# Performance work log

Hardware: AMD Instinct MI355X
Metric: run time of the kernel (lower is better)

The kernel has to match this reference:

```python
import jax, jax.numpy as jnp
import numpy as np

N = 100_000      # nodes
E = 1_600_000    # edges (avg degree 16)
D_IN, D_H, D_OUT = 128, 128, 64


def setup_inputs() -> dict:
    key = jax.random.key(0)
    ks = jax.random.split(key, 6)
    x = jax.random.normal(ks[0], (N, D_IN), jnp.float32)
    edge_index = jax.random.randint(ks[1], (2, E), 0, N, dtype=jnp.int32)
    W1 = jax.random.normal(ks[2], (D_IN, D_H), jnp.float32) / np.sqrt(D_IN)
    b1 = jnp.zeros((D_H,), jnp.float32)
    W2 = jax.random.normal(ks[3], (D_H, D_OUT), jnp.float32) / np.sqrt(D_H)
    b2 = jnp.zeros((D_OUT,), jnp.float32)
    return {"x": x, "edge_index": edge_index, "W1": W1, "b1": b1, "W2": W2, "b2": b2}


def _gcn_layer(x, W, b, src, dst, n_nodes):
    # PyG GCNConv: h = x @ W; symmetric norm with self-loops; scatter-add; + bias
    h = x @ W                                        # [N, D_out]
    deg = jax.ops.segment_sum(jnp.ones_like(dst, jnp.float32), dst,
                              num_segments=n_nodes)  # self-loops => deg >= 1
    dinv = jax.lax.rsqrt(deg)                        # deg^{-1/2}
    norm = dinv[src] * dinv[dst]                     # [E+N]
    msg = h[src] * norm[:, None]                     # gather + scale
    out = jax.ops.segment_sum(msg, dst, num_segments=n_nodes)  # scatter-add
    return out + b


def reference(x, edge_index, W1, b1, W2, b2):
    n = x.shape[0]
    loop = jnp.arange(n, dtype=edge_index.dtype)
    src = jnp.concatenate([edge_index[0], loop])     # add self-loops
    dst = jnp.concatenate([edge_index[1], loop])
    h = _gcn_layer(x, W1, b1, src, dst, n)
    h = jax.nn.relu(h)
    # dropout(p=0.5) is identity in eval mode
    out = _gcn_layer(h, W2, b2, src, dst, n)
    return out
```

## Files before the change

kernel.cpp:

```cpp
#include <hip/hip_runtime.h>
#include <hip/hip_bf16.h>


#define NTHREADS 256
#define BSH 9
#define NBMAX 256

typedef unsigned int uint;
typedef unsigned short ushort;
typedef __attribute__((ext_vector_type(8))) short short8;
typedef __attribute__((ext_vector_type(4))) float floatx4;

__device__ __forceinline__ uint pack_bf16(float a, float b) {
    __hip_bfloat162 h = __float22bfloat162_rn(make_float2(a, b));
    return *reinterpret_cast<uint*>(&h);
}
__device__ __forceinline__ float bf16_lo(uint q) { return __uint_as_float(q << 16); }
__device__ __forceinline__ float bf16_hi(uint q) { return __uint_as_float(q & 0xffff0000u); }

__global__ __launch_bounds__(256) void bucket_hist_kernel(
    const int* __restrict__ dst, int* __restrict__ bcnt, int e, int nb) {
    __shared__ int hist[NBMAX];
    int t = threadIdx.x;
    for (int b = t; b < nb; b += 256) hist[b] = 0;
    __syncthreads();
    int e0 = blockIdx.x * 2048;
#pragma unroll
    for (int v = 0; v < 2; v++) {
        int gi = e0 + t * 8 + v * 4;
        if (gi + 3 < e) {
            int4 d4 = *(const int4*)&dst[gi];
            atomicAdd(&hist[d4.x >> BSH], 1);
            atomicAdd(&hist[d4.y >> BSH], 1);
            atomicAdd(&hist[d4.z >> BSH], 1);
            atomicAdd(&hist[d4.w >> BSH], 1);
        } else {
            for (int j = 0; j < 4; j++)
                if (gi + j < e) atomicAdd(&hist[dst[gi + j] >> BSH], 1);
        }
    }
    __syncthreads();
    for (int b = t; b < nb; b += 256) {
        int v = hist[b];
        if (v) atomicAdd(&bcnt[b], v);
    }
}

__global__ void bucket_scan(const int* __restrict__ bcnt, int* __restrict__ bstart,
                            int* __restrict__ bcursor, int nb) {
    __shared__ int buf[NBMAX];
    int t = threadIdx.x;
    int v = (t < nb) ? bcnt[t] : 0;
    buf[t] = v;
    __syncthreads();
    int x = v;
    for (int off = 1; off < NBMAX; off <<= 1) {
        int y = (t >= off) ? buf[t - off] : 0;
        __syncthreads();
        x += y;
        buf[t] = x;
        __syncthreads();
    }
    if (t < nb) {
        bstart[t] = x - v;
        bcursor[t] = x - v;
    }
}

__global__ __launch_bounds__(256) void partition_kernel(
    const int* __restrict__ src, const int* __restrict__ dst,
    int* __restrict__ bcursor, int2* __restrict__ staged, int e, int nb) {
    __shared__ int eS[2048];
    __shared__ int eD[2048];
    __shared__ int hist[NBMAX];
    __shared__ int base[NBMAX];
    int t = threadIdx.x;
    int e0 = blockIdx.x * 2048;

    for (int b = t; b < nb; b += 256) hist[b] = 0;
    __syncthreads();
#pragma unroll
    for (int v = 0; v < 2; v++) {
        int li = t * 8 + v * 4;
        int gi = e0 + li;
        int4 s4, d4;
        if (gi + 3 < e) {
            s4 = *(const int4*)&src[gi];
            d4 = *(const int4*)&dst[gi];
        } else {
            const int* sp = &src[gi];
            const int* dp = &dst[gi];
            s4.x = (gi + 0 < e) ? sp[0] : 0;  d4.x = (gi + 0 < e) ? dp[0] : -1;
            s4.y = (gi + 1 < e) ? sp[1] : 0;  d4.y = (gi + 1 < e) ? dp[1] : -1;
            s4.z = (gi + 2 < e) ? sp[2] : 0;  d4.z = (gi + 2 < e) ? dp[2] : -1;
            s4.w = (gi + 3 < e) ? sp[3] : 0;  d4.w = (gi + 3 < e) ? dp[3] : -1;
        }
        *(int4*)&eS[li] = s4;
        *(int4*)&eD[li] = d4;
        if (d4.x >= 0) atomicAdd(&hist[d4.x >> BSH], 1);
        if (d4.y >= 0) atomicAdd(&hist[d4.y >> BSH], 1);
        if (d4.z >= 0) atomicAdd(&hist[d4.z >> BSH], 1);
        if (d4.w >= 0) atomicAdd(&hist[d4.w >> BSH], 1);
    }
    __syncthreads();
    for (int b = t; b < nb; b += 256) {
        int v = hist[b];
        base[b] = v ? atomicAdd(&bcursor[b], v) : 0;
        hist[b] = 0;
    }
    __syncthreads();
#pragma unroll
    for (int i = 0; i < 8; i++) {
        int li = t + i * 256;
        int d = eD[li];
        if (d >= 0) {
            int b = d >> BSH;
            int r = atomicAdd(&hist[b], 1);
            staged[base[b] + r] = make_int2(eS[li], d);
        }
    }
}

__global__ __launch_bounds__(256) void fine_count_kernel(
    const int2* __restrict__ staged, const int* __restrict__ bstart,
    const int* __restrict__ bcnt, int4* __restrict__ meta,
    int* __restrict__ startA, float* __restrict__ dinv, int n) {
    __shared__ int lcnt[512];
    __shared__ int tsum[256];
    int b = blockIdx.x;
    int t = threadIdx.x;
    lcnt[t] = 0;
    lcnt[t + 256] = 0;
    __syncthreads();
    int s0 = bstart[b];
    int m = bcnt[b];
    for (int i = t; i < m; i += 256)
        atomicAdd(&lcnt[staged[s0 + i].y & 511], 1);
    __syncthreads();
    int v0 = lcnt[2 * t];
    int v1 = lcnt[2 * t + 1];
    int tot = v0 + v1;
    tsum[t] = tot;
    __syncthreads();
    int x = tot;
    for (int off = 1; off < 256; off <<= 1) {
        int y = (t >= off) ? tsum[t - off] : 0;
        __syncthreads();
        x += y;
        tsum[t] = x;
        __syncthreads();
    }
    int excl = x - tot;
    int node = (b << BSH) + 2 * t;
    if (node < n) {
        float di = rsqrtf((float)v0 + 1.0f);
        startA[node] = s0 + excl;
        dinv[node] = di;
        meta[node] = make_int4(s0 + excl, v0, __float_as_int(di * di), 0);
    }
    if (node + 1 < n) {
        float di = rsqrtf((float)v1 + 1.0f);
        startA[node + 1] = s0 + excl + v0;
        dinv[node + 1] = di;
        meta[node + 1] = make_int4(s0 + excl + v0, v1, __float_as_int(di * di), 0);
    }
}

__global__ __launch_bounds__(256) void fine_fill_kernel(
    const int2* __restrict__ staged, const int* __restrict__ bstart,
    const int* __restrict__ bcnt, const int* __restrict__ startA,
    const float* __restrict__ dinv, int2* __restrict__ rec, int n) {
    __shared__ int lcur[512];
    __shared__ float ldv[512];
    int b = blockIdx.x;
    int t = threadIdx.x;
    int nb0 = b << BSH;
    for (int i = t; i < 512; i += 256) {
        int node = nb0 + i;
        lcur[i] = (node < n) ? startA[node] : 0;
        ldv[i] = (node < n) ? dinv[node] : 0.f;
    }
    __syncthreads();
    int s0 = bstart[b];
    int m = bcnt[b];
    for (int i = t; i < m; i += 256) {
        int2 ed = staged[s0 + i];
        int li = ed.y & 511;
        int pos = atomicAdd(&lcur[li], 1);
        float nw = dinv[ed.x] * ldv[li];
        rec[pos] = make_int2(ed.x, __float_as_int(nw));
    }
}

template <int COLS, bool XF32>
__global__ __launch_bounds__(256) void gemm_mfma(const void* __restrict__ Xv,
                                                 const float* __restrict__ W,
                                                 uint* __restrict__ Cq, int n) {
    __shared__ ushort sX[64 * 128];
    __shared__ ushort sWT[COLS * 128];
    int t = threadIdx.x;
    int rbase = blockIdx.x * 64;

    if (XF32) {
        const float* X = (const float*)Xv;
#pragma unroll
        for (int i = 0; i < 8; i++) {
            int f = t + 256 * i;
            int r = f >> 5;
            int c4 = f & 31;
            float4 v = make_float4(0.f, 0.f, 0.f, 0.f);
            int gr = rbase + r;
            if (gr < n) v = *(const float4*)(X + (size_t)gr * 128 + c4 * 4);
            uint lo = pack_bf16(v.x, v.y);
            uint hi = pack_bf16(v.z, v.w);
            int chunk = c4 >> 1;
            int sub = (c4 & 1) * 4;
            int off = r * 128 + (((chunk ^ (r & 15)) << 3) + sub);
            *(uint2*)&sX[off] = make_uint2(lo, hi);
        }
    } else {
        const ushort* X = (const ushort*)Xv;
#pragma unroll
        for (int i = 0; i < 4; i++) {
            int f = t + 256 * i;
            int r = f >> 4;
            int chunk = f & 15;
            uint4 v = make_uint4(0, 0, 0, 0);
            int gr = rbase + r;
            if (gr < n) v = *(const uint4*)(X + (size_t)gr * 128 + chunk * 8);
            int off = r * 128 + ((chunk ^ (r & 15)) << 3);
            *(uint4*)&sX[off] = v;
        }
    }
    {
        constexpr int UNITS = 64 * (COLS / 4);
        constexpr int PER_T = UNITS / 256;
#pragma unroll
        for (int i = 0; i < PER_T; i++) {
            int u = t + 256 * i;
            int kp = u / (COLS / 4);
            int n4 = u % (COLS / 4);
            int k = kp * 2;
            float4 w0 = *(const float4*)(W + (size_t)k * COLS + n4 * 4);
            float4 w1 = *(const float4*)(W + (size_t)(k + 1) * COLS + n4 * 4);
            int chunk = k >> 3;
            int sub = k & 7;
            const float* a0 = (const float*)&w0;
            const float* a1 = (const float*)&w1;
#pragma unroll
            for (int j = 0; j < 4; j++) {
                int nn = n4 * 4 + j;
                uint pk = pack_bf16(a0[j], a1[j]);
                int off = nn * 128 + (((chunk ^ (nn & 15)) << 3) + sub);
                *(uint*)&sWT[off] = pk;
            }
        }
    }
    __syncthreads();

    int lane = t & 63;
    int wave = t >> 6;
    int m = lane & 15;
    int q = lane >> 4;
    int r0 = wave * 16;

    floatx4 acc[COLS / 16];
#pragma unroll
    for (int c = 0; c < COLS / 16; c++) acc[c] = (floatx4){0.f, 0.f, 0.f, 0.f};

#pragma unroll
    for (int ks = 0; ks < 4; ks++) {
        int rr = r0 + m;
        int ca = (ks * 4 + q) ^ (rr & 15);
        short8 afrag = *(const short8*)&sX[rr * 128 + (ca << 3)];
#pragma unroll
        for (int c = 0; c < COLS / 16; c++) {
            int nn = c * 16 + m;
            int cb = (ks * 4 + q) ^ (nn & 15);
            short8 bfrag = *(const short8*)&sWT[nn * 128 + (cb << 3)];
            acc[c] = __builtin_amdgcn_mfma_f32_16x16x32_bf16(bfrag, afrag, acc[c], 0, 0, 0);
        }
    }

    int gr = rbase + r0 + m;
    if (gr < n) {
#pragma unroll
        for (int c = 0; c < COLS / 16; c++) {
            uint2 pk;
            pk.x = pack_bf16(acc[c][0], acc[c][1]);
            pk.y = pack_bf16(acc[c][2], acc[c][3]);
            *(uint2*)&Cq[(size_t)gr * (COLS / 2) + c * 8 + q * 2] = pk;
        }
    }
}

__global__ __launch_bounds__(256) void aggregate128q(
    const uint* __restrict__ hq, const int2* __restrict__ rec,
    const int4* __restrict__ meta, const float* __restrict__ bias,
    uint* __restrict__ outq, int n) {
    int w = (int)((blockIdx.x * blockDim.x + threadIdx.x) >> 5);
    if (w >= n) return;
    int fl = threadIdx.x & 31;
    const uint2* h2 = (const uint2*)hq;

    int4 mt = meta[w];
    int j0 = mt.x;
    int deg = mt.y;
    float swq = __int_as_float(mt.z);

    uint2 qs = h2[(size_t)w * 32 + fl];
    float a0 = bf16_lo(qs.x) * swq, a1 = bf16_hi(qs.x) * swq;
    float a2 = bf16_lo(qs.y) * swq, a3 = bf16_hi(qs.y) * swq;

    const int2* rp = rec + j0;
    int t = 0;
    for (; t + 8 <= deg; t += 8) {
        uint2 q[8]; float wf[8];
#pragma unroll
        for (int u = 0; u < 8; u++) {
            int2 e = rp[t + u];
            wf[u] = __int_as_float(e.y);
            q[u] = h2[(size_t)e.x * 32 + fl];
        }
#pragma unroll
        for (int u = 0; u < 8; u++) {
            a0 += bf16_lo(q[u].x) * wf[u]; a1 += bf16_hi(q[u].x) * wf[u];
            a2 += bf16_lo(q[u].y) * wf[u]; a3 += bf16_hi(q[u].y) * wf[u];
        }
    }
    for (; t + 2 <= deg; t += 2) {
        int2 e0 = rp[t], e1 = rp[t + 1];
        float w0 = __int_as_float(e0.y), w1 = __int_as_float(e1.y);
        uint2 q0 = h2[(size_t)e0.x * 32 + fl];
        uint2 q1 = h2[(size_t)e1.x * 32 + fl];
        a0 += bf16_lo(q0.x) * w0 + bf16_lo(q1.x) * w1;
        a1 += bf16_hi(q0.x) * w0 + bf16_hi(q1.x) * w1;
        a2 += bf16_lo(q0.y) * w0 + bf16_lo(q1.y) * w1;
        a3 += bf16_hi(q0.y) * w0 + bf16_hi(q1.y) * w1;
    }
    if (t < deg) {
        int2 e = rp[t];
        float wv = __int_as_float(e.y);
        uint2 q = h2[(size_t)e.x * 32 + fl];
        a0 += bf16_lo(q.x) * wv; a1 += bf16_hi(q.x) * wv;
        a2 += bf16_lo(q.y) * wv; a3 += bf16_hi(q.y) * wv;
    }

    float4 bb = *(const float4*)&bias[4 * fl];
    float o0 = fmaxf(a0 + bb.x, 0.f);
    float o1 = fmaxf(a1 + bb.y, 0.f);
    float o2 = fmaxf(a2 + bb.z, 0.f);
    float o3 = fmaxf(a3 + bb.w, 0.f);
    uint2 pk;
    pk.x = pack_bf16(o0, o1);
    pk.y = pack_bf16(o2, o3);
    *(uint2*)&outq[(size_t)w * 64 + fl * 2] = pk;
}

__global__ __launch_bounds__(256) void aggregate64q(
    const ushort* __restrict__ hq, const int2* __restrict__ rec,
    const int4* __restrict__ meta, const float* __restrict__ bias,
    float* __restrict__ out, int n) {
    int w = (int)((blockIdx.x * blockDim.x + threadIdx.x) >> 5);
    if (w >= n) return;
    int fl = threadIdx.x & 31;
    const uint* h2 = (const uint*)hq;

    int4 mt = meta[w];
    int j0 = mt.x;
    int deg = mt.y;
    float swq = __int_as_float(mt.z);

    uint qs = h2[(size_t)w * 32 + fl];
    float a0 = bf16_lo(qs) * swq;
    float a1 = bf16_hi(qs) * swq;

    const int2* rp = rec + j0;
    int t = 0;
    for (; t + 8 <= deg; t += 8) {
        uint q[8]; float wf[8];
#pragma unroll
        for (int u = 0; u < 8; u++) {
            int2 e = rp[t + u];
            wf[u] = __int_as_float(e.y);
            q[u] = h2[(size_t)e.x * 32 + fl];
        }
#pragma unroll
        for (int u = 0; u < 8; u++) {
            a0 += bf16_lo(q[u]) * wf[u];
            a1 += bf16_hi(q[u]) * wf[u];
        }
    }
    for (; t + 2 <= deg; t += 2) {
        int2 e0 = rp[t], e1 = rp[t + 1];
        float w0 = __int_as_float(e0.y), w1 = __int_as_float(e1.y);
        uint q0 = h2[(size_t)e0.x * 32 + fl];
        uint q1 = h2[(size_t)e1.x * 32 + fl];
        a0 += bf16_lo(q0) * w0 + bf16_lo(q1) * w1;
        a1 += bf16_hi(q0) * w0 + bf16_hi(q1) * w1;
    }
    if (t < deg) {
        int2 e = rp[t];
        float wv = __int_as_float(e.y);
        uint q = h2[(size_t)e.x * 32 + fl];
        a0 += bf16_lo(q) * wv;
        a1 += bf16_hi(q) * wv;
    }

    float2 bb = *(const float2*)&bias[2 * fl];
    float2 o;
    o.x = a0 + bb.x;
    o.y = a1 + bb.y;
    ((float2*)out)[(size_t)w * 32 + fl] = o;
}

extern "C" void kernel_launch(void* const* d_in, const int* in_sizes, int n_in,
                              void* d_out, int out_size, void* d_ws, size_t ws_size,
                              hipStream_t stream) {
    const float* x = (const float*)d_in[0];
    const int* edge = (const int*)d_in[1];
    const float* W1 = (const float*)d_in[2];
    const float* b1 = (const float*)d_in[3];
    const float* W2 = (const float*)d_in[4];
    const float* b2 = (const float*)d_in[5];

    const int N = in_sizes[0] / 128;
    const int E = in_sizes[1] / 2;
    const int* src = edge;
    const int* dst = edge + E;
    const int NB = (N + (1 << BSH) - 1) >> BSH;

    char* p = (char*)d_ws;
    int* startA = (int*)p;    p += (size_t)N * 4;
    int* bcnt = (int*)p;      p += NBMAX * 4;
    int* bstart = (int*)p;    p += NBMAX * 4;
    int* bcursor = (int*)p;   p += NBMAX * 4;
    float* dinv = (float*)p;  p += (size_t)N * 4;
    int4* meta = (int4*)p;    p += (size_t)N * 16;
    int2* rec = (int2*)p;     p += (size_t)E * 8;
    uint* hq = (uint*)p;      p += (size_t)N * 64 * 4;
    uint* g = (uint*)p;       p += (size_t)N * 64 * 4;
    ushort* h2q = (ushort*)p; p += (size_t)N * 64 * 2;

    int2* staged = (int2*)g;

    float* out = (float*)d_out;
    const int eblocks = (E + 2047) / 2048;

    (void)hipMemsetAsync(bcnt, 0, NBMAX * 4, stream);
    bucket_hist_kernel<<<eblocks, 256, 0, stream>>>(dst, bcnt, E, NB);
    bucket_scan<<<1, NBMAX, 0, stream>>>(bcnt, bstart, bcursor, NB);
    partition_kernel<<<eblocks, 256, 0, stream>>>(src, dst, bcursor, staged, E, NB);
    fine_count_kernel<<<NB, 256, 0, stream>>>(staged, bstart, bcnt, meta, startA, dinv, N);
    fine_fill_kernel<<<NB, 256, 0, stream>>>(staged, bstart, bcnt, startA, dinv, rec, N);

    const int gblocks = (N + 63) / 64;
    const int ablocks = (N + 7) / 8;

    gemm_mfma<128, true><<<gblocks, 256, 0, stream>>>(x, W1, hq, N);
    aggregate128q<<<ablocks, 256, 0, stream>>>(hq, rec, meta, b1, g, N);

    gemm_mfma<64, false><<<gblocks, 256, 0, stream>>>(g, W2, (uint*)h2q, N);
    aggregate64q<<<ablocks, 256, 0, stream>>>(h2q, rec, meta, b2, out, N);
}
```

Before: 320.2 us.

## Fuse CSR count/fill, drop edge weights, fuse layer-1 aggregation with layer-2 GEMM

Merges the fine count and fill kernels into one, so the CSR build takes one launch and no startA round trip. Edge records shrink from (src, weight) pairs to plain src indices, and the normalisation is recomputed in the aggregation from dinv[src] times the dinv stored in meta. The layer-1 aggregation now also does the W2 matmul: each 512-thread block aggregates 16 nodes into shared memory and runs MFMA on them, which removes the g intermediate and one GEMM launch. The cost is an extra dinv gather per edge, a fused block where only 4 of 8 waves do MFMA, W2 conversion repeated in every block, and a __syncthreads that can stall on the highest-degree node in the block.

```diff
diff --git a/kernel.cpp b/kernel.cpp
--- a/kernel.cpp
+++ b/kernel.cpp
@@ -121,10 +121,10 @@
     }
 }
 
-__global__ __launch_bounds__(256) void fine_count_kernel(
+__global__ __launch_bounds__(256) void fine_csr_kernel(
     const int2* __restrict__ staged, const int* __restrict__ bstart,
     const int* __restrict__ bcnt, int4* __restrict__ meta,
-    int* __restrict__ startA, float* __restrict__ dinv, int n) {
+    float* __restrict__ dinv, int* __restrict__ rec, int n) {
     __shared__ int lcnt[512];
     __shared__ int tsum[256];
     int b = blockIdx.x;
@@ -154,41 +154,22 @@
     int node = (b << BSH) + 2 * t;
     if (node < n) {
         float di = rsqrtf((float)v0 + 1.0f);
-        startA[node] = s0 + excl;
         dinv[node] = di;
-        meta[node] = make_int4(s0 + excl, v0, __float_as_int(di * di), 0);
+        meta[node] = make_int4(s0 + excl, v0, __float_as_int(di), __float_as_int(di * di));
     }
     if (node + 1 < n) {
         float di = rsqrtf((float)v1 + 1.0f);
-        startA[node + 1] = s0 + excl + v0;
         dinv[node + 1] = di;
-        meta[node + 1] = make_int4(s0 + excl + v0, v1, __float_as_int(di * di), 0);
-    }
-}
-
-__global__ __launch_bounds__(256) void fine_fill_kernel(
-    const int2* __restrict__ staged, const int* __restrict__ bstart,
-    const int* __restrict__ bcnt, const int* __restrict__ startA,
-    const float* __restrict__ dinv, int2* __restrict__ rec, int n) {
-    __shared__ int lcur[512];
-    __shared__ float ldv[512];
-    int b = blockIdx.x;
-    int t = threadIdx.x;
-    int nb0 = b << BSH;
-    for (int i = t; i < 512; i += 256) {
-        int node = nb0 + i;
-        lcur[i] = (node < n) ? startA[node] : 0;
-        ldv[i] = (node < n) ? dinv[node] : 0.f;
-    }
-    __syncthreads();
-    int s0 = bstart[b];
-    int m = bcnt[b];
+        meta[node + 1] = make_int4(s0 + excl + v0, v1, __float_as_int(di), __float_as_int(di * di));
+    }
+    lcnt[2 * t] = s0 + excl;
+    lcnt[2 * t + 1] = s0 + excl + v0;
+    __syncthreads();
     for (int i = t; i < m; i += 256) {
         int2 ed = staged[s0 + i];
         int li = ed.y & 511;
-        int pos = atomicAdd(&lcur[li], 1);
-        float nw = dinv[ed.x] * ldv[li];
-        rec[pos] = make_int2(ed.x, __float_as_int(nw));
+        int pos = atomicAdd(&lcnt[li], 1);
+        rec[pos] = ed.x;
     }
 }
 
@@ -294,33 +275,62 @@
     }
 }
 
-__global__ __launch_bounds__(256) void aggregate128q(
-    const uint* __restrict__ hq, const int2* __restrict__ rec,
-    const int4* __restrict__ meta, const float* __restrict__ bias,
-    uint* __restrict__ outq, int n) {
-    int w = (int)((blockIdx.x * blockDim.x + threadIdx.x) >> 5);
-    if (w >= n) return;
-    int fl = threadIdx.x & 31;
+__global__ __launch_bounds__(512) void agg128_mm64(
+    const uint* __restrict__ hq, const int* __restrict__ rec,
+    const int4* __restrict__ meta, const float* __restrict__ dinv,
+    const float* __restrict__ bias, const float* __restrict__ W2,
+    uint* __restrict__ h2q, int n) {
+    __shared__ ushort sWT[64 * 128];
+    __shared__ ushort sg[16 * 128];
+    int t = threadIdx.x;
+
+#pragma unroll
+    for (int i = 0; i < 2; i++) {
+        int u = t + 512 * i;
+        int kp = u >> 4;
+        int n4 = u & 15;
+        int k = kp * 2;
+        float4 w0 = *(const float4*)(W2 + (size_t)k * 64 + n4 * 4);
+        float4 w1 = *(const float4*)(W2 + (size_t)(k + 1) * 64 + n4 * 4);
+        int chunk = k >> 3;
+        int sub = k & 7;
+        const float* a0f = (const float*)&w0;
+        const float* a1f = (const float*)&w1;
+#pragma unroll
+        for (int j = 0; j < 4; j++) {
+            int nn = n4 * 4 + j;
+            uint pk = pack_bf16(a0f[j], a1f[j]);
+            *(uint*)&sWT[nn * 128 + (((chunk ^ (nn & 15)) << 3) + sub)] = pk;
+        }
+    }
+
+    int hw = t >> 5;
+    int fl = t & 31;
+    int nb0 = blockIdx.x * 16;
+    int w = nb0 + hw;
+    bool valid = w < n;
+    int wsafe = valid ? w : 0;
     const uint2* h2 = (const uint2*)hq;
 
-    int4 mt = meta[w];
+    int4 mt = meta[wsafe];
     int j0 = mt.x;
-    int deg = mt.y;
-    float swq = __int_as_float(mt.z);
-
-    uint2 qs = h2[(size_t)w * 32 + fl];
+    int deg = valid ? mt.y : 0;
+    float di = __int_as_float(mt.z);
+    float swq = valid ? __int_as_float(mt.w) : 0.f;
+
+    uint2 qs = h2[(size_t)wsafe * 32 + fl];
     float a0 = bf16_lo(qs.x) * swq, a1 = bf16_hi(qs.x) * swq;
     float a2 = bf16_lo(qs.y) * swq, a3 = bf16_hi(qs.y) * swq;
 
-    const int2* rp = rec + j0;
-    int t = 0;
-    for (; t + 8 <= deg; t += 8) {
+    const int* rp = rec + j0;
+    int tt = 0;
+    for (; tt + 8 <= deg; tt += 8) {
         uint2 q[8]; float wf[8];
 #pragma unroll
         for (int u = 0; u < 8; u++) {
-            int2 e = rp[t + u];
-            wf[u] = __int_as_float(e.y);
-            q[u] = h2[(size_t)e.x * 32 + fl];
+            int s = rp[tt + u];
+            wf[u] = dinv[s] * di;
+            q[u] = h2[(size_t)s * 32 + fl];
         }
 #pragma unroll
         for (int u = 0; u < 8; u++) {
@@ -328,20 +338,20 @@
             a2 += bf16_lo(q[u].y) * wf[u]; a3 += bf16_hi(q[u].y) * wf[u];
         }
     }
-    for (; t + 2 <= deg; t += 2) {
-        int2 e0 = rp[t], e1 = rp[t + 1];
-        float w0 = __int_as_float(e0.y), w1 = __int_as_float(e1.y);
-        uint2 q0 = h2[(size_t)e0.x * 32 + fl];
-        uint2 q1 = h2[(size_t)e1.x * 32 + fl];
-        a0 += bf16_lo(q0.x) * w0 + bf16_lo(q1.x) * w1;
-        a1 += bf16_hi(q0.x) * w0 + bf16_hi(q1.x) * w1;
-        a2 += bf16_lo(q0.y) * w0 + bf16_lo(q1.y) * w1;
-        a3 += bf16_hi(q0.y) * w0 + bf16_hi(q1.y) * w1;
-    }
-    if (t < deg) {
-        int2 e = rp[t];
-        float wv = __int_as_float(e.y);
-        uint2 q = h2[(size_t)e.x * 32 + fl];
+    for (; tt + 2 <= deg; tt += 2) {
+        int s0i = rp[tt], s1i = rp[tt + 1];
+        float w0v = dinv[s0i] * di, w1v = dinv[s1i] * di;
+        uint2 q0 = h2[(size_t)s0i * 32 + fl];
+        uint2 q1 = h2[(size_t)s1i * 32 + fl];
+        a0 += bf16_lo(q0.x) * w0v + bf16_lo(q1.x) * w1v;
+        a1 += bf16_hi(q0.x) * w0v + bf16_hi(q1.x) * w1v;
+        a2 += bf16_lo(q0.y) * w0v + bf16_lo(q1.y) * w1v;
+        a3 += bf16_hi(q0.y) * w0v + bf16_hi(q1.y) * w1v;
+    }
+    if (tt < deg) {
+        int s = rp[tt];
+        float wv = dinv[s] * di;
+        uint2 q = h2[(size_t)s * 32 + fl];
         a0 += bf16_lo(q.x) * wv; a1 += bf16_hi(q.x) * wv;
         a2 += bf16_lo(q.y) * wv; a3 += bf16_hi(q.y) * wv;
     }
@@ -351,39 +361,66 @@
     float o1 = fmaxf(a1 + bb.y, 0.f);
     float o2 = fmaxf(a2 + bb.z, 0.f);
     float o3 = fmaxf(a3 + bb.w, 0.f);
-    uint2 pk;
-    pk.x = pack_bf16(o0, o1);
-    pk.y = pack_bf16(o2, o3);
-    *(uint2*)&outq[(size_t)w * 64 + fl * 2] = pk;
+    {
+        int chunk = fl >> 1;
+        int sub = (fl & 1) * 4;
+        *(uint2*)&sg[hw * 128 + (((chunk ^ hw) << 3) + sub)] =
+            make_uint2(pack_bf16(o0, o1), pack_bf16(o2, o3));
+    }
+    __syncthreads();
+
+    int wave = t >> 6;
+    int lane = t & 63;
+    if (wave < 4) {
+        int m = lane & 15;
+        int q = lane >> 4;
+        floatx4 acc = (floatx4){0.f, 0.f, 0.f, 0.f};
+#pragma unroll
+        for (int ks = 0; ks < 4; ks++) {
+            int ca = (ks * 4 + q) ^ m;
+            short8 afrag = *(const short8*)&sg[m * 128 + (ca << 3)];
+            int nn = wave * 16 + m;
+            int cb = (ks * 4 + q) ^ (nn & 15);
+            short8 bfrag = *(const short8*)&sWT[nn * 128 + (cb << 3)];
+            acc = __builtin_amdgcn_mfma_f32_16x16x32_bf16(bfrag, afrag, acc, 0, 0, 0);
+        }
+        int gr = nb0 + m;
+        if (gr < n) {
+            uint2 pk;
+            pk.x = pack_bf16(acc[0], acc[1]);
+            pk.y = pack_bf16(acc[2], acc[3]);
+            *(uint2*)&h2q[(size_t)gr * 32 + wave * 8 + q * 2] = pk;
+        }
+    }
 }
 
 __global__ __launch_bounds__(256) void aggregate64q(
-    const ushort* __restrict__ hq, const int2* __restrict__ rec,
-    const int4* __restrict__ meta, const float* __restrict__ bias,
-    float* __restrict__ out, int n) {
+    const uint* __restrict__ hq, const int* __restrict__ rec,
+    const int4* __restrict__ meta, const float* __restrict__ dinv,
+    const float* __restrict__ bias, float* __restrict__ out, int n) {
     int w = (int)((blockIdx.x * blockDim.x + threadIdx.x) >> 5);
     if (w >= n) return;
     int fl = threadIdx.x & 31;
-    const uint* h2 = (const uint*)hq;
 
     int4 mt = meta[w];
     int j0 = mt.x;
     int deg = mt.y;
-    float swq = __int_as_float(mt.z);
-
-    uint qs = h2[(size_t)w * 32 + fl];
+    float di = __int_as_float(mt.z);
+    float swq = __int_as_float(mt.w);
+
+    uint qs = hq[(size_t)w * 32 + fl];
     float a0 = bf16_lo(qs) * swq;
     float a1 = bf16_hi(qs) * swq;
 
-    const int2* rp = rec + j0;
+    const int* rp = rec + j0;
     int t = 0;
     for (; t + 8 <= deg; t += 8) {
         uint q[8]; float wf[8];
 #pragma unroll
         for (int u = 0; u < 8; u++) {
-            int2 e = rp[t + u];
-            wf[u] = __int_as_float(e.y);
-            q[u] = h2[(size_t)e.x * 32 + fl];
+            int s = rp[t + u];
+            wf[u] = dinv[s] * di;
+            q[u] = hq[(size_t)s * 32 + fl];
         }
 #pragma unroll
         for (int u = 0; u < 8; u++) {
@@ -392,17 +429,17 @@
         }
     }
     for (; t + 2 <= deg; t += 2) {
-        int2 e0 = rp[t], e1 = rp[t + 1];
-        float w0 = __int_as_float(e0.y), w1 = __int_as_float(e1.y);
-        uint q0 = h2[(size_t)e0.x * 32 + fl];
-        uint q1 = h2[(size_t)e1.x * 32 + fl];
-        a0 += bf16_lo(q0) * w0 + bf16_lo(q1) * w1;
-        a1 += bf16_hi(q0) * w0 + bf16_hi(q1) * w1;
+        int s0i = rp[t], s1i = rp[t + 1];
+        float w0v = dinv[s0i] * di, w1v = dinv[s1i] * di;
+        uint q0 = hq[(size_t)s0i * 32 + fl];
+        uint q1 = hq[(size_t)s1i * 32 + fl];
+        a0 += bf16_lo(q0) * w0v + bf16_lo(q1) * w1v;
+        a1 += bf16_hi(q0) * w0v + bf16_hi(q1) * w1v;
     }
     if (t < deg) {
-        int2 e = rp[t];
-        float wv = __int_as_float(e.y);
-        uint q = h2[(size_t)e.x * 32 + fl];
+        int s = rp[t];
+        float wv = dinv[s] * di;
+        uint q = hq[(size_t)s * 32 + fl];
         a0 += bf16_lo(q) * wv;
         a1 += bf16_hi(q) * wv;
     }
@@ -431,18 +468,15 @@
     const int NB = (N + (1 << BSH) - 1) >> BSH;
 
     char* p = (char*)d_ws;
-    int* startA = (int*)p;    p += (size_t)N * 4;
     int* bcnt = (int*)p;      p += NBMAX * 4;
     int* bstart = (int*)p;    p += NBMAX * 4;
     int* bcursor = (int*)p;   p += NBMAX * 4;
     float* dinv = (float*)p;  p += (size_t)N * 4;
     int4* meta = (int4*)p;    p += (size_t)N * 16;
-    int2* rec = (int2*)p;     p += (size_t)E * 8;
+    int* rec = (int*)p;       p += (size_t)E * 4;
+    int2* staged = (int2*)p;  p += (size_t)E * 8;
     uint* hq = (uint*)p;      p += (size_t)N * 64 * 4;
-    uint* g = (uint*)p;       p += (size_t)N * 64 * 4;
-    ushort* h2q = (ushort*)p; p += (size_t)N * 64 * 2;
-
-    int2* staged = (int2*)g;
+    uint* h2q = (uint*)p;     p += (size_t)N * 32 * 4;
 
     float* out = (float*)d_out;
     const int eblocks = (E + 2047) / 2048;
@@ -451,15 +485,11 @@
     bucket_hist_kernel<<<eblocks, 256, 0, stream>>>(dst, bcnt, E, NB);
     bucket_scan<<<1, NBMAX, 0, stream>>>(bcnt, bstart, bcursor, NB);
     partition_kernel<<<eblocks, 256, 0, stream>>>(src, dst, bcursor, staged, E, NB);
-    fine_count_kernel<<<NB, 256, 0, stream>>>(staged, bstart, bcnt, meta, startA, dinv, N);
-    fine_fill_kernel<<<NB, 256, 0, stream>>>(staged, bstart, bcnt, startA, dinv, rec, N);
+    fine_csr_kernel<<<NB, 256, 0, stream>>>(staged, bstart, bcnt, meta, dinv, rec, N);
 
     const int gblocks = (N + 63) / 64;
-    const int ablocks = (N + 7) / 8;
 
     gemm_mfma<128, true><<<gblocks, 256, 0, stream>>>(x, W1, hq, N);
-    aggregate128q<<<ablocks, 256, 0, stream>>>(hq, rec, meta, b1, g, N);
-
-    gemm_mfma<64, false><<<gblocks, 256, 0, stream>>>(g, W2, (uint*)h2q, N);
-    aggregate64q<<<ablocks, 256, 0, stream>>>(h2q, rec, meta, b2, out, N);
-}
+    agg128_mm64<<<(N + 15) / 16, 512, 0, stream>>>(hq, rec, meta, dinv, b1, W2, h2q, N);
+    aggregate64q<<<(N + 7) / 8, 256, 0, stream>>>(h2q, rec, meta, dinv, b2, out, N);
+}
```

Result: faster. 298.7 us (-6.7%).
